# Kernel optimization log

Measured on AMD Instinct MI355X. Metric: run time of the kernel, lower is better.

Reference implementation:

```python
import jax, jax.numpy as jnp
import numpy as np


def setup_inputs() -> dict:
    key = jax.random.key(0)
    ks = jax.random.split(key, 6)
    B, C, S, E = 8, 16, 512, 256
    wscale = (2.0 / (E + E)) ** 0.5  # xavier_normal for [E, E] fan_in=fan_out=E
    return {
        "query": jax.random.normal(ks[0], (B, C, S, E), dtype=jnp.float32),
        "key": jax.random.normal(ks[1], (B, C, S, E), dtype=jnp.float32),
        "value": jax.random.normal(ks[2], (B, C, S, E), dtype=jnp.float32),
        "q_proj_weight": jax.random.normal(ks[3], (C, E, E), dtype=jnp.float32) * wscale,
        "k_proj_weight": jax.random.normal(ks[4], (C, E, E), dtype=jnp.float32) * wscale,
        "v_proj_weight": jax.random.normal(ks[5], (C, E, E), dtype=jnp.float32) * wscale,
        "q_proj_bias": jnp.zeros((C, 1, E), dtype=jnp.float32),
        "k_proj_bias": jnp.zeros((C, 1, E), dtype=jnp.float32),
        "v_proj_bias": jnp.zeros((C, 1, E), dtype=jnp.float32),
    }


def reference(query, key, value, q_proj_weight, k_proj_weight, v_proj_weight,
              q_proj_bias, k_proj_bias, v_proj_bias):
    E = query.shape[-1]
    # Per-cycle projection + bias + ReLU.  b=batch, c=cycle, s/t=seq, e/f=embed
    q = jax.nn.relu(jnp.einsum("bcse,cef->bcsf", query, q_proj_weight) + q_proj_bias)
    k = jax.nn.relu(jnp.einsum("bcse,cef->bcsf", key, k_proj_weight) + k_proj_bias)
    v = jax.nn.relu(jnp.einsum("bcse,cef->bcsf", value, v_proj_weight) + v_proj_bias)
    q = q * (float(E) ** -0.5)
    attn = jax.nn.softmax(jnp.einsum("bcse,bcte->bcst", q, k), axis=-1)
    out = jnp.einsum("bcst,bcte->bcse", attn, v)
    return out
```

## Files before the change

### kernel.cpp

```cpp
#include <hip/hip_runtime.h>

constexpr int BATCH = 8;
constexpr int CYC   = 16;
constexpr int SEQ   = 512;
constexpr int EMB   = 256;

typedef __attribute__((ext_vector_type(8))) short bf16x8;
typedef __attribute__((ext_vector_type(4))) float f32x4;

__device__ __forceinline__ unsigned short f2bf(float x) {
    unsigned int u = __float_as_uint(x);
    u += 0x7fffu + ((u >> 16) & 1u);
    return (unsigned short)(u >> 16);
}
__device__ __forceinline__ unsigned int pk2(float lo, float hi) {
    return (unsigned int)f2bf(lo) | ((unsigned int)f2bf(hi) << 16);
}
__device__ __forceinline__ f32x4 mfma16(bf16x8 a, bf16x8 b, f32x4 c) {
    return __builtin_amdgcn_mfma_f32_16x16x32_bf16(a, b, c, 0, 0, 0);
}
__device__ __forceinline__ void gll16(const void* g, void* l) {
    __builtin_amdgcn_global_load_lds(
        (const __attribute__((address_space(1))) void*)g,
        (__attribute__((address_space(3))) void*)l, 16, 0, 0);
}
union BCast { int4 i; bf16x8 v; };

__global__ __launch_bounds__(256) void wt_kernel(
    const float* __restrict__ Wq, const float* __restrict__ Wk,
    const float* __restrict__ Wv,
    unsigned short* __restrict__ Tq, unsigned short* __restrict__ Tk,
    unsigned short* __restrict__ Tv)
{
    __shared__ float tile[64][65];
    const int z = blockIdx.z;
    const int which = z >> 4, c = z & 15;
    const float* W = which == 0 ? Wq : which == 1 ? Wk : Wv;
    unsigned short* Wt = which == 0 ? Tq : which == 1 ? Tk : Tv;
    const int e0 = blockIdx.x * 64;
    const int f0 = blockIdx.y * 64;
    const float* Wc = W + (size_t)c * EMB * EMB;
    unsigned short* Wtc = Wt + (size_t)c * EMB * EMB;
    const int t = threadIdx.x;
    {
        const int er = t >> 4;
        const int fc = (t & 15) * 4;
        for (int i = 0; i < 4; ++i) {
            const float4 v = *(const float4*)(Wc + (size_t)(e0 + er + i * 16) * EMB + f0 + fc);
            tile[er + i * 16][fc + 0] = v.x;
            tile[er + i * 16][fc + 1] = v.y;
            tile[er + i * 16][fc + 2] = v.z;
            tile[er + i * 16][fc + 3] = v.w;
        }
    }
    __syncthreads();
    {
        const int fr = t >> 4;
        const int ec = (t & 15) * 4;
        for (int i = 0; i < 4; ++i) {
            const int f = fr + i * 16;
            ushort4 o;
            o.x = f2bf(tile[ec + 0][f]);
            o.y = f2bf(tile[ec + 1][f]);
            o.z = f2bf(tile[ec + 2][f]);
            o.w = f2bf(tile[ec + 3][f]);
            *(ushort4*)(Wtc + (size_t)(f0 + f) * EMB + e0 + ec) = o;
        }
    }
}

__global__ __launch_bounds__(256, 3) void proj_kernel(
    const float* __restrict__ Xq, const float* __restrict__ Xk,
    const float* __restrict__ Xv,
    const unsigned short* __restrict__ Wq, const unsigned short* __restrict__ Wk,
    const unsigned short* __restrict__ Wv,
    const float* __restrict__ Bq, const float* __restrict__ Bk,
    const float* __restrict__ Bv,
    unsigned short* __restrict__ Yq, unsigned short* __restrict__ Yk,
    unsigned short* __restrict__ Yv)
{
    __shared__ float          As[2][64 * 32];
    __shared__ unsigned short Bs[2][256 * 32];

    const int z = blockIdx.z;
    const float* X = z == 0 ? Xq : z == 1 ? Xk : Xv;
    const unsigned short* Wt = z == 0 ? Wq : z == 1 ? Wk : Wv;
    const float* bias = z == 0 ? Bq : z == 1 ? Bk : Bv;
    unsigned short* Y = z == 0 ? Yq : z == 1 ? Yk : Yv;
    const float scale = z == 0 ? 0.0625f : 1.0f;

    const int bc = blockIdx.x;
    const int c  = bc & (CYC - 1);
    const int m0 = blockIdx.y * 64;
    const float* Xb = X + (size_t)bc * SEQ * EMB;
    const unsigned short* Wc = Wt + (size_t)c * EMB * EMB;
    const float* bb = bias + (size_t)c * EMB;
    unsigned short* Yb = Y + (size_t)bc * SEQ * EMB;

    const int tid  = threadIdx.x;
    const int lane = tid & 63, w = tid >> 6;
    const int ln   = lane & 15, quad = lane >> 4;
    const int wu   = __builtin_amdgcn_readfirstlane(w);

    const int arow = lane >> 3;
    const int achk = (lane & 7) ^ arow;
    const int brow = lane >> 2;
    const int gch  = (lane & 3) ^ ((lane >> 3) & 3);
    const int s8    = ln & 7;
    const int bslot = quad ^ ((ln >> 1) & 3);

    f32x4 acc[4][4];
    for (int i = 0; i < 4; ++i)
        for (int j = 0; j < 4; ++j) acc[i][j] = (f32x4){0.f, 0.f, 0.f, 0.f};

    auto stage = [&](int kk, int b) {
        const int k0 = kk * 32;
#pragma unroll
        for (int j = 0; j < 2; ++j) {
            const int r0 = wu * 16 + j * 8;
            gll16(Xb + (size_t)(m0 + r0 + arow) * EMB + k0 + achk * 4,
                  &As[b][r0 * 32]);
        }
#pragma unroll
        for (int j = 0; j < 4; ++j) {
            const int r0 = wu * 64 + j * 16;
            gll16(Wc + (size_t)(r0 + brow) * EMB + k0 + gch * 8,
                  &Bs[b][r0 * 32]);
        }
    };

    stage(0, 0);
#pragma unroll
    for (int kk = 0; kk < 8; ++kk) {
        const int cur = kk & 1;
        if (kk < 7) {
            stage(kk + 1, cur ^ 1);
            asm volatile("s_waitcnt vmcnt(6)" ::: "memory");
        } else {
            asm volatile("s_waitcnt vmcnt(0)" ::: "memory");
        }
        __builtin_amdgcn_s_barrier();
        __builtin_amdgcn_sched_barrier(0);

        bf16x8 af[4], bfv[4];
#pragma unroll
        for (int i = 0; i < 4; ++i) {
            const float* ar = &As[cur][(i * 16 + ln) * 32];
            const float4 f0 = *(const float4*)(ar + ((2 * quad)     ^ s8) * 4);
            const float4 f1 = *(const float4*)(ar + ((2 * quad + 1) ^ s8) * 4);
            BCast u;
            u.i.x = pk2(f0.x, f0.y); u.i.y = pk2(f0.z, f0.w);
            u.i.z = pk2(f1.x, f1.y); u.i.w = pk2(f1.z, f1.w);
            af[i] = u.v;
        }
#pragma unroll
        for (int j = 0; j < 4; ++j)
            bfv[j] = *(const bf16x8*)&Bs[cur][(w * 64 + j * 16 + ln) * 32 + bslot * 8];
#pragma unroll
        for (int i = 0; i < 4; ++i)
#pragma unroll
            for (int j = 0; j < 4; ++j)
                acc[i][j] = mfma16(af[i], bfv[j], acc[i][j]);

        __builtin_amdgcn_sched_barrier(0);
        asm volatile("s_waitcnt lgkmcnt(0)" ::: "memory");
        __builtin_amdgcn_s_barrier();
    }

    float bvj[4];
#pragma unroll
    for (int j = 0; j < 4; ++j) bvj[j] = bb[w * 64 + j * 16 + ln];

    if (z != 2) {
        unsigned short* ep = (unsigned short*)&As[0][0] + w * 1152;
        for (int i = 0; i < 4; ++i) {
            for (int j = 0; j < 4; ++j)
                for (int r = 0; r < 4; ++r)
                    ep[(quad * 4 + r) * 72 + j * 16 + ln] =
                        f2bf(fmaxf(acc[i][j][r] + bvj[j], 0.f) * scale);
            __syncthreads();
            for (int h = 0; h < 2; ++h) {
                const int cid = lane + h * 64;
                const int row = cid >> 3, ch = cid & 7;
                *(bf16x8*)&Yb[(size_t)(m0 + i * 16 + row) * EMB + w * 64 + ch * 8] =
                    *(const bf16x8*)&ep[row * 72 + ch * 8];
            }
            __syncthreads();
        }
    } else {
        for (int j = 0; j < 4; ++j) {
            const int fg = w * 64 + j * 16 + ln;
            for (int i = 0; i < 4; ++i) {
                const int mb = m0 + i * 16 + quad * 4;
                ushort4 u;
                u.x = f2bf(fmaxf(acc[i][j][0] + bvj[j], 0.f) * scale);
                u.y = f2bf(fmaxf(acc[i][j][1] + bvj[j], 0.f) * scale);
                u.z = f2bf(fmaxf(acc[i][j][2] + bvj[j], 0.f) * scale);
                u.w = f2bf(fmaxf(acc[i][j][3] + bvj[j], 0.f) * scale);
                *(ushort4*)&Yb[(size_t)fg * SEQ + mb] = u;
            }
        }
    }
}

__global__ __launch_bounds__(256, 3) void attn_kernel(
    const unsigned short* __restrict__ Qp, const unsigned short* __restrict__ Kp,
    const unsigned short* __restrict__ Vt, float* __restrict__ Out)
{
    __shared__ unsigned short Vs[2][256 * 32];
    __shared__ unsigned short Ps[64][40];
    const int bc = blockIdx.x;
    const int qt = blockIdx.y;
    const unsigned short* Qb = Qp + (size_t)bc * SEQ * EMB;
    const unsigned short* Kb = Kp + (size_t)bc * SEQ * EMB;
    const unsigned short* Vb = Vt + (size_t)bc * SEQ * EMB;
    float* Ob = Out + (size_t)bc * SEQ * EMB;

    const int tid  = threadIdx.x;
    const int lane = tid & 63, w = tid >> 6;
    const int ln   = lane & 15, quad = lane >> 4;
    const int wu   = __builtin_amdgcn_readfirstlane(w);
    const int brow = lane >> 2;
    const int gch  = (lane & 3) ^ ((lane >> 3) & 3);
    const int vslot = quad ^ ((ln >> 1) & 3);

    bf16x8 qf[8];
    const int qrow = qt * 64 + w * 16 + ln;
#pragma unroll
    for (int ke = 0; ke < 8; ++ke)
        qf[ke] = *(const bf16x8*)(Qb + (size_t)qrow * EMB + ke * 32 + quad * 8);

    f32x4 of[16];
    for (int n = 0; n < 16; ++n) of[n] = (f32x4){0.f, 0.f, 0.f, 0.f};
    float lsum[4] = {0.f, 0.f, 0.f, 0.f};

    auto stageV = [&](int tt, int b) {
        const int t0 = tt * 32;
#pragma unroll
        for (int j = 0; j < 4; ++j) {
            const int r0 = wu * 64 + j * 16;
            gll16(Vb + (size_t)(r0 + brow) * SEQ + t0 + gch * 8,
                  &Vs[b][r0 * 32]);
        }
    };

    stageV(0, 0);

    const unsigned short* Kq = Kb + (size_t)ln * EMB + quad * 8;

    for (int tt = 0; tt < 16; ++tt) {
        const int cur = tt & 1;
        const int t0 = tt * 32;

        f32x4 sf0 = (f32x4){0.f,0.f,0.f,0.f}, sf1 = (f32x4){0.f,0.f,0.f,0.f};
        const unsigned short* K0 = Kq + (size_t)t0 * EMB;
#pragma unroll
        for (int ke = 0; ke < 8; ++ke) {
            bf16x8 b0 = *(const bf16x8*)(K0 + ke * 32);
            bf16x8 b1 = *(const bf16x8*)(K0 + (size_t)16 * EMB + ke * 32);
            sf0 = mfma16(qf[ke], b0, sf0);
            sf1 = mfma16(qf[ke], b1, sf1);
        }

        float p0[4], p1[4];
#pragma unroll
        for (int r = 0; r < 4; ++r) {
            p0[r] = __expf(sf0[r]);
            p1[r] = __expf(sf1[r]);
            lsum[r] += p0[r] + p1[r];
        }
#pragma unroll
        for (int r = 0; r < 4; ++r) {
            Ps[w * 16 + quad * 4 + r][ln]      = f2bf(p0[r]);
            Ps[w * 16 + quad * 4 + r][16 + ln] = f2bf(p1[r]);
        }

        if (tt < 15) {
            stageV(tt + 1, cur ^ 1);
            asm volatile("s_waitcnt vmcnt(4) lgkmcnt(0)" ::: "memory");
        } else {
            asm volatile("s_waitcnt vmcnt(0) lgkmcnt(0)" ::: "memory");
        }
        __builtin_amdgcn_s_barrier();
        __builtin_amdgcn_sched_barrier(0);

        bf16x8 af = *(const bf16x8*)&Ps[w * 16 + ln][quad * 8];
#pragma unroll
        for (int n = 0; n < 16; ++n) {
            bf16x8 bv = *(const bf16x8*)&Vs[cur][(n * 16 + ln) * 32 + vslot * 8];
            of[n] = mfma16(af, bv, of[n]);
        }
        __builtin_amdgcn_sched_barrier(0);
        asm volatile("s_waitcnt lgkmcnt(0)" ::: "memory");
        __builtin_amdgcn_s_barrier();
    }

    for (int off = 1; off < 16; off <<= 1)
        for (int r = 0; r < 4; ++r)
            lsum[r] += __shfl_xor(lsum[r], off, 64);
    float inv[4];
    for (int r = 0; r < 4; ++r) inv[r] = 1.0f / lsum[r];
    const int mbase = qt * 64 + w * 16 + quad * 4;
    for (int n = 0; n < 16; ++n)
        for (int r = 0; r < 4; ++r)
            Ob[(size_t)(mbase + r) * EMB + n * 16 + ln] = of[n][r] * inv[r];
}

extern "C" void kernel_launch(void* const* d_in, const int* in_sizes, int n_in,
                              void* d_out, int out_size, void* d_ws, size_t ws_size,
                              hipStream_t stream) {
    const float* query = (const float*)d_in[0];
    const float* key_  = (const float*)d_in[1];
    const float* value = (const float*)d_in[2];
    const float* wq = (const float*)d_in[3];
    const float* wk = (const float*)d_in[4];
    const float* wv = (const float*)d_in[5];
    const float* bq = (const float*)d_in[6];
    const float* bk = (const float*)d_in[7];
    const float* bv = (const float*)d_in[8];
    float* out = (float*)d_out;

    char* ws = (char*)d_ws;
    const size_t wsz = (size_t)CYC * EMB * EMB * sizeof(unsigned short);
    const size_t psz = (size_t)BATCH * CYC * SEQ * EMB * sizeof(unsigned short);
    unsigned short* Wtq = (unsigned short*)(ws);
    unsigned short* Wtk = (unsigned short*)(ws + wsz);
    unsigned short* Wtv = (unsigned short*)(ws + 2 * wsz);
    unsigned short* Qp  = (unsigned short*)(ws + 3 * wsz);
    unsigned short* Kp  = (unsigned short*)(ws + 3 * wsz + psz);
    unsigned short* Vtp = (unsigned short*)(ws + 3 * wsz + 2 * psz);

    const dim3 tb(256);
    wt_kernel<<<dim3(4, 4, 3 * CYC), tb, 0, stream>>>(wq, wk, wv, Wtq, Wtk, Wtv);

    proj_kernel<<<dim3(BATCH * CYC, SEQ / 64, 3), tb, 0, stream>>>(
        query, key_, value, Wtq, Wtk, Wtv, bq, bk, bv, Qp, Kp, Vtp);

    attn_kernel<<<dim3(BATCH * CYC, SEQ / 64), tb, 0, stream>>>(Qp, Kp, Vtp, out);
}
```

Before: 411.5 us.

## Stage K and V tiles through LDS via register prefetch instead of direct loads

The attention kernel now cooperatively loads each 32-row K tile and V tile into registers one iteration ahead, writes them to padded single-buffered LDS arrays, and reads the MFMA operands from LDS. This replaces per-wave direct global reads of K, which the four waves of a block each repeated, and the async global_load_lds double buffer for V. The goal is to cut redundant global K traffic, but it adds register pressure from kreg/vreg, drops the occupancy hint of 3 blocks, and adds an extra barrier per iteration.

```diff
diff --git a/kernel.cpp b/kernel.cpp
--- a/kernel.cpp
+++ b/kernel.cpp
@@ -203,11 +203,12 @@
     }
 }
 
-__global__ __launch_bounds__(256, 3) void attn_kernel(
+__global__ __launch_bounds__(256) void attn_kernel(
     const unsigned short* __restrict__ Qp, const unsigned short* __restrict__ Kp,
     const unsigned short* __restrict__ Vt, float* __restrict__ Out)
 {
-    __shared__ unsigned short Vs[2][256 * 32];
+    __shared__ unsigned short Ks[32][264];
+    __shared__ unsigned short Vs[256][40];
     __shared__ unsigned short Ps[64][40];
     const int bc = blockIdx.x;
     const int qt = blockIdx.y;
@@ -219,10 +220,6 @@
     const int tid  = threadIdx.x;
     const int lane = tid & 63, w = tid >> 6;
     const int ln   = lane & 15, quad = lane >> 4;
-    const int wu   = __builtin_amdgcn_readfirstlane(w);
-    const int brow = lane >> 2;
-    const int gch  = (lane & 3) ^ ((lane >> 3) & 3);
-    const int vslot = quad ^ ((ln >> 1) & 3);
 
     bf16x8 qf[8];
     const int qrow = qt * 64 + w * 16 + ln;
@@ -234,30 +231,45 @@
     for (int n = 0; n < 16; ++n) of[n] = (f32x4){0.f, 0.f, 0.f, 0.f};
     float lsum[4] = {0.f, 0.f, 0.f, 0.f};
 
-    auto stageV = [&](int tt, int b) {
+    bf16x8 kreg[4], vreg[4];
+    auto loadKV = [&](int tt) {
         const int t0 = tt * 32;
 #pragma unroll
-        for (int j = 0; j < 4; ++j) {
-            const int r0 = wu * 64 + j * 16;
-            gll16(Vb + (size_t)(r0 + brow) * SEQ + t0 + gch * 8,
-                  &Vs[b][r0 * 32]);
+        for (int i = 0; i < 4; ++i) {
+            const int idx = tid + i * 256;
+            const int r = idx >> 5, c8 = (idx & 31) * 8;
+            kreg[i] = *(const bf16x8*)(Kb + (size_t)(t0 + r) * EMB + c8);
+        }
+#pragma unroll
+        for (int i = 0; i < 4; ++i) {
+            const int idx = tid + i * 256;
+            const int e = idx >> 2, c8 = (idx & 3) * 8;
+            vreg[i] = *(const bf16x8*)(Vb + (size_t)e * SEQ + t0 + c8);
         }
     };
-
-    stageV(0, 0);
-
-    const unsigned short* Kq = Kb + (size_t)ln * EMB + quad * 8;
+    loadKV(0);
 
     for (int tt = 0; tt < 16; ++tt) {
-        const int cur = tt & 1;
-        const int t0 = tt * 32;
+#pragma unroll
+        for (int i = 0; i < 4; ++i) {
+            const int idx = tid + i * 256;
+            const int r = idx >> 5, c8 = (idx & 31) * 8;
+            *(bf16x8*)&Ks[r][c8] = kreg[i];
+        }
+#pragma unroll
+        for (int i = 0; i < 4; ++i) {
+            const int idx = tid + i * 256;
+            const int e = idx >> 2, c8 = (idx & 3) * 8;
+            *(bf16x8*)&Vs[e][c8] = vreg[i];
+        }
+        __syncthreads();
+        if (tt < 15) loadKV(tt + 1);
 
         f32x4 sf0 = (f32x4){0.f,0.f,0.f,0.f}, sf1 = (f32x4){0.f,0.f,0.f,0.f};
-        const unsigned short* K0 = Kq + (size_t)t0 * EMB;
 #pragma unroll
         for (int ke = 0; ke < 8; ++ke) {
-            bf16x8 b0 = *(const bf16x8*)(K0 + ke * 32);
-            bf16x8 b1 = *(const bf16x8*)(K0 + (size_t)16 * EMB + ke * 32);
+            bf16x8 b0 = *(const bf16x8*)&Ks[ln][ke * 32 + quad * 8];
+            bf16x8 b1 = *(const bf16x8*)&Ks[16 + ln][ke * 32 + quad * 8];
             sf0 = mfma16(qf[ke], b0, sf0);
             sf1 = mfma16(qf[ke], b1, sf1);
         }
@@ -274,25 +286,15 @@
             Ps[w * 16 + quad * 4 + r][ln]      = f2bf(p0[r]);
             Ps[w * 16 + quad * 4 + r][16 + ln] = f2bf(p1[r]);
         }
-
-        if (tt < 15) {
-            stageV(tt + 1, cur ^ 1);
-            asm volatile("s_waitcnt vmcnt(4) lgkmcnt(0)" ::: "memory");
-        } else {
-            asm volatile("s_waitcnt vmcnt(0) lgkmcnt(0)" ::: "memory");
-        }
-        __builtin_amdgcn_s_barrier();
-        __builtin_amdgcn_sched_barrier(0);
+        __syncthreads();
 
         bf16x8 af = *(const bf16x8*)&Ps[w * 16 + ln][quad * 8];
 #pragma unroll
         for (int n = 0; n < 16; ++n) {
-            bf16x8 bv = *(const bf16x8*)&Vs[cur][(n * 16 + ln) * 32 + vslot * 8];
+            bf16x8 bv = *(const bf16x8*)&Vs[n * 16 + ln][quad * 8];
             of[n] = mfma16(af, bv, of[n]);
         }
-        __builtin_amdgcn_sched_barrier(0);
-        asm volatile("s_waitcnt lgkmcnt(0)" ::: "memory");
-        __builtin_amdgcn_s_barrier();
+        __syncthreads();
     }
 
     for (int off = 1; off < 16; off <<= 1)
```

Result: faster. 335.0 us (-18.6%).
